# Kernel tuning notes

Hardware: AMD Instinct MI355X
Metric: run time of the kernel (lower is better)

## Reference

```python
import jax, jax.numpy as jnp
import numpy as np

N_NODES = 100000
N_EDGES = 1600000
D_FEAT = 128
N_CLASS = 40
K_HOPS = 2  # nlayers


def setup_inputs() -> dict:
    key = jax.random.key(0)
    k1, k2, k3, k4, k5 = jax.random.split(key, 5)
    src = jax.random.randint(k1, (N_EDGES,), 0, N_NODES)
    dst = jax.random.randint(k2, (N_EDGES,), 0, N_NODES)
    features = jax.random.normal(k3, (N_NODES, D_FEAT), dtype=jnp.float32)
    # positive edge weights (EdgeWeightNorm requires nonnegative)
    edge_weight = jax.random.uniform(k4, (N_EDGES,), dtype=jnp.float32, minval=0.1, maxval=1.0)
    W = jax.random.normal(k5, (D_FEAT, N_CLASS), dtype=jnp.float32) / np.float32(np.sqrt(D_FEAT))
    b = jnp.zeros((N_CLASS,), dtype=jnp.float32)
    return {"features": features, "src": src, "dst": dst,
            "edge_weight": edge_weight, "W": W, "b": b}


def reference(features, src, dst, edge_weight, W, b):
    """SGConv (DGL) with edge_weight: EdgeWeightNorm('both') then k SpMM hops, then fc."""
    n = features.shape[0]
    # EdgeWeightNorm('both'): w_ij / sqrt(out_deg_w(src_i) * in_deg_w(dst_j))
    out_deg = jax.ops.segment_sum(edge_weight, src, num_segments=n)  # weighted out-degree
    in_deg = jax.ops.segment_sum(edge_weight, dst, num_segments=n)   # weighted in-degree
    w = edge_weight * jax.lax.rsqrt(out_deg[src]) * jax.lax.rsqrt(in_deg[dst])  # [E]
    h = features
    for _ in range(K_HOPS):
        # message = h[src] * w ; aggregate = scatter-sum over dst
        h = jax.ops.segment_sum(h[src] * w[:, None], dst, num_segments=n)  # [N, D]
    return h @ W + b  # fc projection [N, C]
```

## Files before the change

### kernel.cpp

```cpp
#include <hip/hip_runtime.h>

#define N_NODES 100000
#define N_EDGES 1600000
#define D_FEAT  128
#define N_CLASS 40
#define ELL_CAP 48

#define QS  10239.6875f
#define DQ  9.765923e-5f
#define FSC  2048.0f
#define FINV (1.0f/2048.0f)
#define CNT_SHIFT 20
#define W_MASK ((1u << CNT_SHIFT) - 1u)

#define RSZ 16000
#define NR 7
#define SLICES 32
#define EPS (N_EDGES/SLICES)
#define HB (NR*SLICES)

#define GEMM2_T ((N_NODES/2)*(N_CLASS/4))
#define GEMM2_B ((GEMM2_T + 1023)/1024)

#define NCH 5

__device__ __forceinline__ float bf_lo(unsigned int u) { return __uint_as_float(u << 16); }
__device__ __forceinline__ float bf_hi(unsigned int u) { return __uint_as_float(u & 0xFFFF0000u); }
__device__ __forceinline__ unsigned int bf_pack2(float a, float b) {
    unsigned int ua = __float_as_uint(a), ub = __float_as_uint(b);
    ua = (ua + 0x7FFFu + ((ua >> 16) & 1u)) >> 16;
    ub = (ub + 0x7FFFu + ((ub >> 16) & 1u)) & 0xFFFF0000u;
    return ua | ub;
}

__global__ __launch_bounds__(1024) void mega1_kernel(
    const int* __restrict__ src, const int* __restrict__ dst, const float* __restrict__ ew,
    const float* __restrict__ f, const float* __restrict__ W,
    unsigned int* __restrict__ dhist, unsigned int* __restrict__ shist,
    unsigned int* __restrict__ g0)
{
    __shared__ unsigned int smem[RSZ];
    const int b = blockIdx.x;
    const int tid = threadIdx.x;

    if (b < 2 * HB) {
        const bool isDst = (b < HB);
        const int b2 = isDst ? b : b - HB;
        const int* idxarr = isDst ? dst : src;
        unsigned int* outh = isDst ? dhist : shist;
        int r = b2 / SLICES, s = b2 - r * SLICES;
        int nb = r * RSZ;
        unsigned int lim = (unsigned int)min(RSZ, N_NODES - nb);
        for (int i = tid; i < RSZ; i += 1024) smem[i] = 0u;
        __syncthreads();
        int e0 = s * EPS;
        const int2*  idx2 = (const int2*)(idxarr + e0);
        const float2* ew2 = (const float2*)(ew + e0);
        const unsigned int cbit = isDst ? (1u << CNT_SHIFT) : 0u;
        for (int i = tid; i < EPS / 2; i += 1024) {
            int2 ii = idx2[i];
            float2 ww = ew2[i];
            unsigned int r0 = (unsigned int)(ii.x - nb);
            unsigned int r1 = (unsigned int)(ii.y - nb);
            if (r0 < lim) atomicAdd(&smem[r0], cbit | (unsigned int)(ww.x * FSC + 0.5f));
            if (r1 < lim) atomicAdd(&smem[r1], cbit | (unsigned int)(ww.y * FSC + 0.5f));
        }
        __syncthreads();
        unsigned int* o = outh + (size_t)b2 * RSZ;
        for (int i = tid; i < RSZ; i += 1024) o[i] = smem[i];
    } else {
        float* Ws = (float*)smem;
        for (int i = tid; i < D_FEAT * N_CLASS; i += 1024) Ws[i] = W[i];
        __syncthreads();
        int idx = (b - 2 * HB) * 1024 + tid;
        if (idx >= GEMM2_T) return;
        int n2 = idx / (N_CLASS / 4);
        int c4i = idx - n2 * (N_CLASS / 4);
        int c4 = c4i * 4;
        int n0 = n2 * 2;
        const float* fr0 = f + (size_t)n0 * D_FEAT;
        const float* fr1 = fr0 + D_FEAT;
        float4 acc0 = {0.f, 0.f, 0.f, 0.f};
        float4 acc1 = {0.f, 0.f, 0.f, 0.f};
#pragma unroll 1
        for (int kq = 0; kq < D_FEAT; kq += 4) {
            float4 fv0 = *(const float4*)(fr0 + kq);
            float4 fv1 = *(const float4*)(fr1 + kq);
#pragma unroll
            for (int j = 0; j < 4; ++j) {
                float fa = (j == 0) ? fv0.x : (j == 1) ? fv0.y : (j == 2) ? fv0.z : fv0.w;
                float fb = (j == 0) ? fv1.x : (j == 1) ? fv1.y : (j == 2) ? fv1.z : fv1.w;
                const float4 wv = *(const float4*)&Ws[(kq + j) * N_CLASS + c4];
                acc0.x = fmaf(fa, wv.x, acc0.x); acc0.y = fmaf(fa, wv.y, acc0.y);
                acc0.z = fmaf(fa, wv.z, acc0.z); acc0.w = fmaf(fa, wv.w, acc0.w);
                acc1.x = fmaf(fb, wv.x, acc1.x); acc1.y = fmaf(fb, wv.y, acc1.y);
                acc1.z = fmaf(fb, wv.z, acc1.z); acc1.w = fmaf(fb, wv.w, acc1.w);
            }
        }
        uint2 p0, p1;
        p0.x = bf_pack2(acc0.x, acc0.y); p0.y = bf_pack2(acc0.z, acc0.w);
        p1.x = bf_pack2(acc1.x, acc1.y); p1.y = bf_pack2(acc1.z, acc1.w);
        *(uint2*)&g0[(size_t)n0 * (N_CLASS / 2) + c4i * 2] = p0;
        *(uint2*)&g0[(size_t)(n0 + 1) * (N_CLASS / 2) + c4i * 2] = p1;
    }
}

__global__ void scan_kernel(const unsigned int* __restrict__ dhist,
                            const unsigned int* __restrict__ shist,
                            unsigned char* __restrict__ base8, int* __restrict__ cnt,
                            float* __restrict__ rs_out, float* __restrict__ rs_in,
                            unsigned int* __restrict__ ell)
{
    int n = blockIdx.x * 256 + threadIdx.x;
    if (n >= N_NODES) return;
    int r = n / RSZ, off = n - r * RSZ;
    const unsigned int* dp = dhist + (size_t)r * SLICES * RSZ + off;
    const unsigned int* sp = shist + (size_t)r * SLICES * RSZ + off;
    unsigned char* b8 = base8 + (size_t)r * SLICES * RSZ + off;
    unsigned int ow = 0, iw = 0, run = 0;
#pragma unroll
    for (int s = 0; s < SLICES; ++s) {
        unsigned int dv = dp[(size_t)s * RSZ];
        ow += sp[(size_t)s * RSZ];
        b8[(size_t)s * RSZ] = (unsigned char)run;
        run += dv >> CNT_SHIFT;
        iw += dv & W_MASK;
    }
    rs_out[n] = ow ? rsqrtf((float)ow * FINV) : 0.f;
    rs_in[n]  = iw ? rsqrtf((float)iw * FINV) : 0.f;
    cnt[n] = (int)run;
    int k  = min((int)run, ELL_CAP);
    int k4 = min((k + 3) & ~3, ELL_CAP);
    unsigned int* row = ell + (size_t)n * ELL_CAP;
    for (int i = k; i < k4; ++i) row[i] = 0u;
}

__global__ __launch_bounds__(1024) void fill_kernel(
    const int* __restrict__ src, const int* __restrict__ dst, const float* __restrict__ ew,
    const unsigned char* __restrict__ base8, const float* __restrict__ rs_out,
    unsigned int* __restrict__ ell)
{
    __shared__ unsigned int lds[RSZ];
    const int b = blockIdx.x;
    const int tid = threadIdx.x;
    int r = b / SLICES, s = b - r * SLICES;
    int nb = r * RSZ;
    unsigned int lim = (unsigned int)min(RSZ, N_NODES - nb);
    const unsigned int* bp = (const unsigned int*)(base8 + (size_t)b * RSZ);
    for (int i = tid; i < RSZ / 4; i += 1024) {
        unsigned int v = bp[i];
        lds[4 * i]     = v & 255u;
        lds[4 * i + 1] = (v >> 8) & 255u;
        lds[4 * i + 2] = (v >> 16) & 255u;
        lds[4 * i + 3] = v >> 24;
    }
    __syncthreads();
    int e0 = s * EPS;
    const int2*  d2  = (const int2*)(dst + e0);
    const int2*  s2  = (const int2*)(src + e0);
    const float2* w2 = (const float2*)(ew + e0);
    for (int i = tid; i < EPS / 2; i += 1024) {
        int2 dd = d2[i];
        int2 ss = s2[i];
        float2 ww = w2[i];
#pragma unroll
        for (int j = 0; j < 2; ++j) {
            int d  = (j == 0) ? dd.x : dd.y;
            int sn = (j == 0) ? ss.x : ss.y;
            float w = (j == 0) ? ww.x : ww.y;
            unsigned int rr = (unsigned int)(d - nb);
            if (rr < lim) {
                unsigned int slot = atomicAdd(&lds[rr], 1u);
                if (slot < ELL_CAP) {
                    int q = (int)(w * rs_out[sn] * QS + 0.5f);
                    q = q > 32767 ? 32767 : q;
                    ell[(size_t)d * ELL_CAP + slot] = ((unsigned int)sn << 15) | (unsigned int)q;
                }
            }
        }
    }
}

__global__ void hop_kernel(const unsigned int* __restrict__ ell, const int* __restrict__ cnt,
                           const float* __restrict__ rs_in, const unsigned int* __restrict__ gin,
                           void* __restrict__ gout, const float* __restrict__ bias)
{
    int t = blockIdx.x * 256 + threadIdx.x;
    if (t >= N_NODES * NCH) return;
    int n = t / NCH;
    int c8 = t - n * NCH;
    int k = min(cnt[n], ELL_CAP);
    k = (k + 3) & ~3;
    const uint4* row4 = (const uint4*)(ell + (size_t)n * ELL_CAP);
    const uint4* gin4 = (const uint4*)gin;
    float a0 = 0.f, a1 = 0.f, a2 = 0.f, a3 = 0.f, a4 = 0.f, a5 = 0.f, a6 = 0.f, a7 = 0.f;
    for (int i = 0; i < k; i += 4) {
        uint4 v = row4[i >> 2];
#pragma unroll
        for (int j = 0; j < 4; ++j) {
            unsigned int e = (j == 0) ? v.x : (j == 1) ? v.y : (j == 2) ? v.z : v.w;
            float w = (float)(e & 32767u) * DQ;
            uint4 gv = gin4[(size_t)(e >> 15) * NCH + c8];
            a0 = fmaf(w, bf_lo(gv.x), a0); a1 = fmaf(w, bf_hi(gv.x), a1);
            a2 = fmaf(w, bf_lo(gv.y), a2); a3 = fmaf(w, bf_hi(gv.y), a3);
            a4 = fmaf(w, bf_lo(gv.z), a4); a5 = fmaf(w, bf_hi(gv.z), a5);
            a6 = fmaf(w, bf_lo(gv.w), a6); a7 = fmaf(w, bf_hi(gv.w), a7);
        }
    }
    float sc = rs_in[n];
    a0 *= sc; a1 *= sc; a2 *= sc; a3 *= sc; a4 *= sc; a5 *= sc; a6 *= sc; a7 *= sc;
    if (bias) {
        const float4 b0 = *(const float4*)&bias[c8 * 8];
        const float4 b1 = *(const float4*)&bias[c8 * 8 + 4];
        float4 o0 = {a0 + b0.x, a1 + b0.y, a2 + b0.z, a3 + b0.w};
        float4 o1 = {a4 + b1.x, a5 + b1.y, a6 + b1.z, a7 + b1.w};
        float* op = (float*)gout + (size_t)n * N_CLASS + c8 * 8;
        *(float4*)op = o0;
        *(float4*)(op + 4) = o1;
    } else {
        uint4 p;
        p.x = bf_pack2(a0, a1);
        p.y = bf_pack2(a2, a3);
        p.z = bf_pack2(a4, a5);
        p.w = bf_pack2(a6, a7);
        ((uint4*)gout)[(size_t)n * NCH + c8] = p;
    }
}

extern "C" void kernel_launch(void* const* d_in, const int* in_sizes, int n_in,
                              void* d_out, int out_size, void* d_ws, size_t ws_size,
                              hipStream_t stream) {
    const float* features = (const float*)d_in[0];
    const int*   src      = (const int*)d_in[1];
    const int*   dst      = (const int*)d_in[2];
    const float* ew       = (const float*)d_in[3];
    const float* W        = (const float*)d_in[4];
    const float* b        = (const float*)d_in[5];
    float*       out      = (float*)d_out;

    char* ws = (char*)d_ws;
    unsigned int* dhist = (unsigned int*)ws;  ws += (size_t)HB * RSZ * 4;
    unsigned int* shist = (unsigned int*)ws;  ws += (size_t)HB * RSZ * 4;
    unsigned char* base8 = (unsigned char*)ws; ws += (size_t)HB * RSZ;
    int*   cnt    = (int*)ws;    ws += (size_t)N_NODES * 4;
    float* rs_out = (float*)ws;  ws += (size_t)N_NODES * 4;
    float* rs_in  = (float*)ws;  ws += (size_t)N_NODES * 4;
    unsigned int* ell = (unsigned int*)ws; ws += (size_t)N_NODES * ELL_CAP * 4;
    unsigned int* g0  = (unsigned int*)ws;
    unsigned int* g1  = dhist;

    const int B = 256;

    mega1_kernel<<<2 * HB + GEMM2_B, 1024, 0, stream>>>(
        src, dst, ew, features, W, dhist, shist, g0);
    scan_kernel<<<(N_NODES + B - 1) / B, B, 0, stream>>>(
        dhist, shist, base8, cnt, rs_out, rs_in, ell);
    fill_kernel<<<HB, 1024, 0, stream>>>(src, dst, ew, base8, rs_out, ell);

    const int HOP_BLOCKS = (N_NODES * NCH + B - 1) / B;
    hop_kernel<<<HOP_BLOCKS, B, 0, stream>>>(ell, cnt, rs_in, g0, (void*)g1, nullptr);
    hop_kernel<<<HOP_BLOCKS, B, 0, stream>>>(ell, cnt, rs_in, g1, (void*)out, b);
}
```

Baseline: 262.1 us.

## Replace sliced LDS histograms and scan with global float atomics for degrees and ELL fill

```diff
diff --git a/kernel.cpp b/kernel.cpp
--- a/kernel.cpp
+++ b/kernel.cpp
@@ -8,21 +8,14 @@
 
 #define QS  10239.6875f
 #define DQ  9.765923e-5f
-#define FSC  2048.0f
-#define FINV (1.0f/2048.0f)
-#define CNT_SHIFT 20
-#define W_MASK ((1u << CNT_SHIFT) - 1u)
 
-#define RSZ 16000
-#define NR 7
-#define SLICES 32
-#define EPS (N_EDGES/SLICES)
-#define HB (NR*SLICES)
+#define NCH 5
 
 #define GEMM2_T ((N_NODES/2)*(N_CLASS/4))
 #define GEMM2_B ((GEMM2_T + 1023)/1024)
 
-#define NCH 5
+#define QUADS (N_EDGES/4)
+#define DEG_B ((QUADS + 1023)/1024)
 
 __device__ __forceinline__ float bf_lo(unsigned int u) { return __uint_as_float(u << 16); }
 __device__ __forceinline__ float bf_hi(unsigned int u) { return __uint_as_float(u & 0xFFFF0000u); }
@@ -36,160 +29,97 @@
 __global__ __launch_bounds__(1024) void mega1_kernel(
     const int* __restrict__ src, const int* __restrict__ dst, const float* __restrict__ ew,
     const float* __restrict__ f, const float* __restrict__ W,
-    unsigned int* __restrict__ dhist, unsigned int* __restrict__ shist,
+    float* __restrict__ outw, float* __restrict__ inw,
     unsigned int* __restrict__ g0)
 {
-    __shared__ unsigned int smem[RSZ];
+    __shared__ float Ws[D_FEAT * N_CLASS];
     const int b = blockIdx.x;
     const int tid = threadIdx.x;
 
-    if (b < 2 * HB) {
-        const bool isDst = (b < HB);
-        const int b2 = isDst ? b : b - HB;
-        const int* idxarr = isDst ? dst : src;
-        unsigned int* outh = isDst ? dhist : shist;
-        int r = b2 / SLICES, s = b2 - r * SLICES;
-        int nb = r * RSZ;
-        unsigned int lim = (unsigned int)min(RSZ, N_NODES - nb);
-        for (int i = tid; i < RSZ; i += 1024) smem[i] = 0u;
-        __syncthreads();
-        int e0 = s * EPS;
-        const int2*  idx2 = (const int2*)(idxarr + e0);
-        const float2* ew2 = (const float2*)(ew + e0);
-        const unsigned int cbit = isDst ? (1u << CNT_SHIFT) : 0u;
-        for (int i = tid; i < EPS / 2; i += 1024) {
-            int2 ii = idx2[i];
-            float2 ww = ew2[i];
-            unsigned int r0 = (unsigned int)(ii.x - nb);
-            unsigned int r1 = (unsigned int)(ii.y - nb);
-            if (r0 < lim) atomicAdd(&smem[r0], cbit | (unsigned int)(ww.x * FSC + 0.5f));
-            if (r1 < lim) atomicAdd(&smem[r1], cbit | (unsigned int)(ww.y * FSC + 0.5f));
+    if (b < DEG_B) {
+        int q = b * 1024 + tid;
+        if (q < QUADS) {
+            int4   s4 = ((const int4*)src)[q];
+            int4   d4 = ((const int4*)dst)[q];
+            float4 w4 = ((const float4*)ew)[q];
+            atomicAdd(&outw[s4.x], w4.x);
+            atomicAdd(&outw[s4.y], w4.y);
+            atomicAdd(&outw[s4.z], w4.z);
+            atomicAdd(&outw[s4.w], w4.w);
+            atomicAdd(&inw[d4.x], w4.x);
+            atomicAdd(&inw[d4.y], w4.y);
+            atomicAdd(&inw[d4.z], w4.z);
+            atomicAdd(&inw[d4.w], w4.w);
         }
-        __syncthreads();
-        unsigned int* o = outh + (size_t)b2 * RSZ;
-        for (int i = tid; i < RSZ; i += 1024) o[i] = smem[i];
-    } else {
-        float* Ws = (float*)smem;
-        for (int i = tid; i < D_FEAT * N_CLASS; i += 1024) Ws[i] = W[i];
-        __syncthreads();
-        int idx = (b - 2 * HB) * 1024 + tid;
-        if (idx >= GEMM2_T) return;
-        int n2 = idx / (N_CLASS / 4);
-        int c4i = idx - n2 * (N_CLASS / 4);
-        int c4 = c4i * 4;
-        int n0 = n2 * 2;
-        const float* fr0 = f + (size_t)n0 * D_FEAT;
-        const float* fr1 = fr0 + D_FEAT;
-        float4 acc0 = {0.f, 0.f, 0.f, 0.f};
-        float4 acc1 = {0.f, 0.f, 0.f, 0.f};
+        return;
+    }
+    for (int i = tid; i < D_FEAT * N_CLASS; i += 1024) Ws[i] = W[i];
+    __syncthreads();
+    int idx = (b - DEG_B) * 1024 + tid;
+    if (idx >= GEMM2_T) return;
+    int n2 = idx / (N_CLASS / 4);
+    int c4i = idx - n2 * (N_CLASS / 4);
+    int c4 = c4i * 4;
+    int n0 = n2 * 2;
+    const float* fr0 = f + (size_t)n0 * D_FEAT;
+    const float* fr1 = fr0 + D_FEAT;
+    float4 acc0 = {0.f, 0.f, 0.f, 0.f};
+    float4 acc1 = {0.f, 0.f, 0.f, 0.f};
 #pragma unroll 1
-        for (int kq = 0; kq < D_FEAT; kq += 4) {
-            float4 fv0 = *(const float4*)(fr0 + kq);
-            float4 fv1 = *(const float4*)(fr1 + kq);
+    for (int kq = 0; kq < D_FEAT; kq += 4) {
+        float4 fv0 = *(const float4*)(fr0 + kq);
+        float4 fv1 = *(const float4*)(fr1 + kq);
 #pragma unroll
-            for (int j = 0; j < 4; ++j) {
-                float fa = (j == 0) ? fv0.x : (j == 1) ? fv0.y : (j == 2) ? fv0.z : fv0.w;
-                float fb = (j == 0) ? fv1.x : (j == 1) ? fv1.y : (j == 2) ? fv1.z : fv1.w;
-                const float4 wv = *(const float4*)&Ws[(kq + j) * N_CLASS + c4];
-                acc0.x = fmaf(fa, wv.x, acc0.x); acc0.y = fmaf(fa, wv.y, acc0.y);
-                acc0.z = fmaf(fa, wv.z, acc0.z); acc0.w = fmaf(fa, wv.w, acc0.w);
-                acc1.x = fmaf(fb, wv.x, acc1.x); acc1.y = fmaf(fb, wv.y, acc1.y);
-                acc1.z = fmaf(fb, wv.z, acc1.z); acc1.w = fmaf(fb, wv.w, acc1.w);
-            }
+        for (int j = 0; j < 4; ++j) {
+            float fa = (j == 0) ? fv0.x : (j == 1) ? fv0.y : (j == 2) ? fv0.z : fv0.w;
+            float fb = (j == 0) ? fv1.x : (j == 1) ? fv1.y : (j == 2) ? fv1.z : fv1.w;
+            const float4 wv = *(const float4*)&Ws[(kq + j) * N_CLASS + c4];
+            acc0.x = fmaf(fa, wv.x, acc0.x); acc0.y = fmaf(fa, wv.y, acc0.y);
+            acc0.z = fmaf(fa, wv.z, acc0.z); acc0.w = fmaf(fa, wv.w, acc0.w);
+            acc1.x = fmaf(fb, wv.x, acc1.x); acc1.y = fmaf(fb, wv.y, acc1.y);
+            acc1.z = fmaf(fb, wv.z, acc1.z); acc1.w = fmaf(fb, wv.w, acc1.w);
         }
-        uint2 p0, p1;
-        p0.x = bf_pack2(acc0.x, acc0.y); p0.y = bf_pack2(acc0.z, acc0.w);
-        p1.x = bf_pack2(acc1.x, acc1.y); p1.y = bf_pack2(acc1.z, acc1.w);
-        *(uint2*)&g0[(size_t)n0 * (N_CLASS / 2) + c4i * 2] = p0;
-        *(uint2*)&g0[(size_t)(n0 + 1) * (N_CLASS / 2) + c4i * 2] = p1;
     }
-}
-
-__global__ void scan_kernel(const unsigned int* __restrict__ dhist,
-                            const unsigned int* __restrict__ shist,
-                            unsigned char* __restrict__ base8, int* __restrict__ cnt,
-                            float* __restrict__ rs_out, float* __restrict__ rs_in,
-                            unsigned int* __restrict__ ell)
-{
-    int n = blockIdx.x * 256 + threadIdx.x;
-    if (n >= N_NODES) return;
-    int r = n / RSZ, off = n - r * RSZ;
-    const unsigned int* dp = dhist + (size_t)r * SLICES * RSZ + off;
-    const unsigned int* sp = shist + (size_t)r * SLICES * RSZ + off;
-    unsigned char* b8 = base8 + (size_t)r * SLICES * RSZ + off;
-    unsigned int ow = 0, iw = 0, run = 0;
-#pragma unroll
-    for (int s = 0; s < SLICES; ++s) {
-        unsigned int dv = dp[(size_t)s * RSZ];
-        ow += sp[(size_t)s * RSZ];
-        b8[(size_t)s * RSZ] = (unsigned char)run;
-        run += dv >> CNT_SHIFT;
-        iw += dv & W_MASK;
-    }
-    rs_out[n] = ow ? rsqrtf((float)ow * FINV) : 0.f;
-    rs_in[n]  = iw ? rsqrtf((float)iw * FINV) : 0.f;
-    cnt[n] = (int)run;
-    int k  = min((int)run, ELL_CAP);
-    int k4 = min((k + 3) & ~3, ELL_CAP);
-    unsigned int* row = ell + (size_t)n * ELL_CAP;
-    for (int i = k; i < k4; ++i) row[i] = 0u;
+    uint2 p0, p1;
+    p0.x = bf_pack2(acc0.x, acc0.y); p0.y = bf_pack2(acc0.z, acc0.w);
+    p1.x = bf_pack2(acc1.x, acc1.y); p1.y = bf_pack2(acc1.z, acc1.w);
+    *(uint2*)&g0[(size_t)n0 * (N_CLASS / 2) + c4i * 2] = p0;
+    *(uint2*)&g0[(size_t)(n0 + 1) * (N_CLASS / 2) + c4i * 2] = p1;
 }
 
 __global__ __launch_bounds__(1024) void fill_kernel(
     const int* __restrict__ src, const int* __restrict__ dst, const float* __restrict__ ew,
-    const unsigned char* __restrict__ base8, const float* __restrict__ rs_out,
+    const float* __restrict__ outw, unsigned int* __restrict__ cnt,
     unsigned int* __restrict__ ell)
 {
-    __shared__ unsigned int lds[RSZ];
-    const int b = blockIdx.x;
-    const int tid = threadIdx.x;
-    int r = b / SLICES, s = b - r * SLICES;
-    int nb = r * RSZ;
-    unsigned int lim = (unsigned int)min(RSZ, N_NODES - nb);
-    const unsigned int* bp = (const unsigned int*)(base8 + (size_t)b * RSZ);
-    for (int i = tid; i < RSZ / 4; i += 1024) {
-        unsigned int v = bp[i];
-        lds[4 * i]     = v & 255u;
-        lds[4 * i + 1] = (v >> 8) & 255u;
-        lds[4 * i + 2] = (v >> 16) & 255u;
-        lds[4 * i + 3] = v >> 24;
-    }
-    __syncthreads();
-    int e0 = s * EPS;
-    const int2*  d2  = (const int2*)(dst + e0);
-    const int2*  s2  = (const int2*)(src + e0);
-    const float2* w2 = (const float2*)(ew + e0);
-    for (int i = tid; i < EPS / 2; i += 1024) {
-        int2 dd = d2[i];
-        int2 ss = s2[i];
-        float2 ww = w2[i];
+    int q = blockIdx.x * 1024 + threadIdx.x;
+    if (q >= QUADS) return;
+    int4   s4 = ((const int4*)src)[q];
+    int4   d4 = ((const int4*)dst)[q];
+    float4 w4 = ((const float4*)ew)[q];
 #pragma unroll
-        for (int j = 0; j < 2; ++j) {
-            int d  = (j == 0) ? dd.x : dd.y;
-            int sn = (j == 0) ? ss.x : ss.y;
-            float w = (j == 0) ? ww.x : ww.y;
-            unsigned int rr = (unsigned int)(d - nb);
-            if (rr < lim) {
-                unsigned int slot = atomicAdd(&lds[rr], 1u);
-                if (slot < ELL_CAP) {
-                    int q = (int)(w * rs_out[sn] * QS + 0.5f);
-                    q = q > 32767 ? 32767 : q;
-                    ell[(size_t)d * ELL_CAP + slot] = ((unsigned int)sn << 15) | (unsigned int)q;
-                }
-            }
+    for (int j = 0; j < 4; ++j) {
+        int   sn = (j == 0) ? s4.x : (j == 1) ? s4.y : (j == 2) ? s4.z : s4.w;
+        int   d  = (j == 0) ? d4.x : (j == 1) ? d4.y : (j == 2) ? d4.z : d4.w;
+        float w  = (j == 0) ? w4.x : (j == 1) ? w4.y : (j == 2) ? w4.z : w4.w;
+        unsigned int slot = atomicAdd(&cnt[d], 1u);
+        if (slot < ELL_CAP) {
+            int qv = (int)(w * rsqrtf(outw[sn]) * QS + 0.5f);
+            qv = qv > 32767 ? 32767 : qv;
+            ell[(size_t)d * ELL_CAP + slot] = ((unsigned int)sn << 15) | (unsigned int)qv;
         }
     }
 }
 
-__global__ void hop_kernel(const unsigned int* __restrict__ ell, const int* __restrict__ cnt,
-                           const float* __restrict__ rs_in, const unsigned int* __restrict__ gin,
+__global__ void hop_kernel(const unsigned int* __restrict__ ell, const unsigned int* __restrict__ cnt,
+                           const float* __restrict__ inw, const unsigned int* __restrict__ gin,
                            void* __restrict__ gout, const float* __restrict__ bias)
 {
     int t = blockIdx.x * 256 + threadIdx.x;
     if (t >= N_NODES * NCH) return;
     int n = t / NCH;
     int c8 = t - n * NCH;
-    int k = min(cnt[n], ELL_CAP);
+    int k = min((int)cnt[n], ELL_CAP);
     k = (k + 3) & ~3;
     const uint4* row4 = (const uint4*)(ell + (size_t)n * ELL_CAP);
     const uint4* gin4 = (const uint4*)gin;
@@ -207,7 +137,8 @@
             a6 = fmaf(w, bf_lo(gv.w), a6); a7 = fmaf(w, bf_hi(gv.w), a7);
         }
     }
-    float sc = rs_in[n];
+    float iw = inw[n];
+    float sc = iw > 0.f ? rsqrtf(iw) : 0.f;
     a0 *= sc; a1 *= sc; a2 *= sc; a3 *= sc; a4 *= sc; a5 *= sc; a6 *= sc; a7 *= sc;
     if (bias) {
         const float4 b0 = *(const float4*)&bias[c8 * 8];
@@ -239,25 +170,22 @@
     float*       out      = (float*)d_out;
 
     char* ws = (char*)d_ws;
-    unsigned int* dhist = (unsigned int*)ws;  ws += (size_t)HB * RSZ * 4;
-    unsigned int* shist = (unsigned int*)ws;  ws += (size_t)HB * RSZ * 4;
-    unsigned char* base8 = (unsigned char*)ws; ws += (size_t)HB * RSZ;
-    int*   cnt    = (int*)ws;    ws += (size_t)N_NODES * 4;
-    float* rs_out = (float*)ws;  ws += (size_t)N_NODES * 4;
-    float* rs_in  = (float*)ws;  ws += (size_t)N_NODES * 4;
-    unsigned int* ell = (unsigned int*)ws; ws += (size_t)N_NODES * ELL_CAP * 4;
-    unsigned int* g0  = (unsigned int*)ws;
-    unsigned int* g1  = dhist;
+    unsigned int* cnt  = (unsigned int*)ws;  ws += (size_t)N_NODES * 4;
+    float*        outw = (float*)ws;         ws += (size_t)N_NODES * 4;
+    float*        inw  = (float*)ws;         ws += (size_t)N_NODES * 4;
+    unsigned int* ell  = (unsigned int*)ws;  ws += (size_t)N_NODES * ELL_CAP * 4;
+    unsigned int* g0   = (unsigned int*)ws;  ws += (size_t)N_NODES * NCH * 16;
+    unsigned int* g1   = (unsigned int*)ws;
+
+    const size_t zero_bytes = (size_t)N_NODES * 4 * 3 + (size_t)N_NODES * ELL_CAP * 4;
+    hipMemsetAsync(d_ws, 0, zero_bytes, stream);
+
+    mega1_kernel<<<DEG_B + GEMM2_B, 1024, 0, stream>>>(
+        src, dst, ew, features, W, outw, inw, g0);
+    fill_kernel<<<DEG_B, 1024, 0, stream>>>(src, dst, ew, outw, cnt, ell);
 
     const int B = 256;
-
-    mega1_kernel<<<2 * HB + GEMM2_B, 1024, 0, stream>>>(
-        src, dst, ew, features, W, dhist, shist, g0);
-    scan_kernel<<<(N_NODES + B - 1) / B, B, 0, stream>>>(
-        dhist, shist, base8, cnt, rs_out, rs_in, ell);
-    fill_kernel<<<HB, 1024, 0, stream>>>(src, dst, ew, base8, rs_out, ell);
-
     const int HOP_BLOCKS = (N_NODES * NCH + B - 1) / B;
-    hop_kernel<<<HOP_BLOCKS, B, 0, stream>>>(ell, cnt, rs_in, g0, (void*)g1, nullptr);
-    hop_kernel<<<HOP_BLOCKS, B, 0, stream>>>(ell, cnt, rs_in, g1, (void*)out, b);
+    hop_kernel<<<HOP_BLOCKS, B, 0, stream>>>(ell, cnt, inw, g0, (void*)g1, nullptr);
+    hop_kernel<<<HOP_BLOCKS, B, 0, stream>>>(ell, cnt, inw, g1, (void*)out, b);
 }
```

Result: slower. 423.4 us (+61.6%).
